# Kernel tuning notes

Hardware: AMD Instinct MI355X
Metric: run time of the kernel (lower is better)

Reference implementation:

```python
import jax, jax.numpy as jnp
import numpy as np

NUM_HEADS = 12

def setup_inputs() -> dict:
    key = jax.random.key(0)
    k1, k2 = jax.random.split(key)
    X = jax.random.normal(k1, (2, 2048, 768), dtype=jnp.float32)
    # torch nn.Linear(dim, 2*dim, bias=False) weight has shape [2*dim, dim]
    W_qkv = jax.random.normal(k2, (1536, 768), dtype=jnp.float32) * (768 ** -0.5)
    return {"X": X, "W_qkv": W_qkv}

def reference(X, W_qkv):
    B, N, C = X.shape
    H = NUM_HEADS
    hd = C // H
    scale = hd ** -0.5
    # qkv: [B, N, 2, H, hd]
    qkv = (X @ W_qkv.T).reshape(B, N, 2, H, hd)
    q = jnp.transpose(qkv[:, :, 0], (0, 2, 1, 3))  # [B, H, N, hd]
    k = jnp.transpose(qkv[:, :, 1], (0, 2, 1, 3))  # [B, H, N, hd]
    attn = jnp.einsum('bhnd,bhmd->bhnm', q, k) * scale  # [B, H, N, N]
    # dropout p=0 -> identity; double sum over heads and keys
    scores = attn.sum(axis=1).sum(axis=-1)  # [B, N]
    return scores
```

## Files before the change

### kernel.cpp

```cpp
#include <hip/hip_runtime.h>


#define DIM 768
#define BATCH 2
#define SEQ 2048


__global__ void colsum_part(const float* __restrict__ X, float* __restrict__ part) {
    int b  = blockIdx.x >> 6;
    int ch = blockIdx.x & 63;
    int i  = threadIdx.x;
    const float4* base = (const float4*)(X + ((size_t)b * SEQ + (size_t)ch * 32) * DIM) + i;
    float4 a = {0.f, 0.f, 0.f, 0.f};
    #pragma unroll 8
    for (int n = 0; n < 32; ++n) {
        float4 x = base[n * 192];
        a.x += x.x; a.y += x.y; a.z += x.z; a.w += x.w;
    }
    ((float4*)(part + (size_t)(b * 64 + ch) * DIM))[i] = a;
}

__global__ void v_kernel(const float* __restrict__ W, const float* __restrict__ part,
                         float* __restrict__ v) {
    __shared__ alignas(16) float xs[DIM];
    int bi = blockIdx.x;
    int b = bi >= 48;
    int tid = threadIdx.x;
    for (int d = tid; d < DIM; d += 256) {
        float s = 0.f;
        #pragma unroll 8
        for (int ch = 0; ch < 64; ++ch)
            s += part[(size_t)(b * 64 + ch) * DIM + d];
        xs[d] = s;
    }
    __syncthreads();
    int gw = bi * 4 + (tid >> 6);
    int lane = tid & 63;
    const float4* xs4 = (const float4*)xs;
    #pragma unroll
    for (int k = 0; k < 4; ++k) {
        int o = gw * 4 + k;
        int c = o - b * DIM;
        const float4* wr = (const float4*)(W + (size_t)(DIM + c) * DIM);
        float acc = 0.f;
        #pragma unroll
        for (int j = 0; j < 3; ++j) {
            float4 a = wr[lane + 64 * j];
            float4 s = xs4[lane + 64 * j];
            acc += a.x * s.x + a.y * s.y + a.z * s.z + a.w * s.w;
        }
        #pragma unroll
        for (int off = 32; off; off >>= 1)
            acc += __shfl_down(acc, off, 64);
        if (lane == 0) v[o] = acc;
    }
}

__global__ void t_part(const float* __restrict__ W, const float* __restrict__ v,
                       float* __restrict__ tp) {
    int bi = blockIdx.x;
    int b = bi / 24;
    int rem = bi % 24;
    int cs = rem / 3;
    int dch = rem % 3;
    int d = dch * 256 + threadIdx.x;
    const float* vb = v + b * DIM;
    float acc = 0.f;
    int c0 = cs * 96;
    #pragma unroll 8
    for (int c = c0; c < c0 + 96; ++c)
        acc += W[(size_t)c * DIM + d] * vb[c];
    tp[(size_t)(b * 8 + cs) * DIM + d] = acc;
}

__global__ void scores_k(const float* __restrict__ X, const float* __restrict__ tp,
                         float* __restrict__ out) {
    __shared__ alignas(16) float ft[DIM];
    int r0 = blockIdx.x * 4;
    int b = r0 >> 11;
    int tid = threadIdx.x;
    if (tid < 192) {
        const float4* base = (const float4*)(tp + (size_t)b * 8 * DIM) + tid;
        float4 s = {0.f, 0.f, 0.f, 0.f};
        #pragma unroll
        for (int cs = 0; cs < 8; ++cs) {
            float4 a = base[cs * 192];
            s.x += a.x; s.y += a.y; s.z += a.z; s.w += a.w;
        }
        ((float4*)ft)[tid] = s;
    }
    __syncthreads();
    int r = r0 + (tid >> 6);
    int lane = tid & 63;
    const float4* xr = (const float4*)(X + (size_t)r * DIM);
    const float4* t4 = (const float4*)ft;
    float acc = 0.f;
    #pragma unroll
    for (int j = 0; j < 3; ++j) {
        float4 a = xr[lane + 64 * j];
        float4 s = t4[lane + 64 * j];
        acc += a.x * s.x + a.y * s.y + a.z * s.z + a.w * s.w;
    }
    #pragma unroll
    for (int off = 32; off; off >>= 1)
        acc += __shfl_down(acc, off, 64);
    if (lane == 0) out[r] = acc * 0.125f;
}

extern "C" void kernel_launch(void* const* d_in, const int* in_sizes, int n_in,
                              void* d_out, int out_size, void* d_ws, size_t ws_size,
                              hipStream_t stream) {
    const float* X = (const float*)d_in[0];
    const float* W = (const float*)d_in[1];
    float* out = (float*)d_out;
    float* ws = (float*)d_ws;
    float* part = ws;
    float* v    = ws + 2 * 64 * DIM;
    float* tp   = v + 2 * DIM;

    colsum_part<<<128, 192, 0, stream>>>(X, part);
    v_kernel  <<<96, 256, 0, stream>>>(W, part, v);
    t_part    <<<48, 256, 0, stream>>>(W, v, tp);
    scores_k  <<<1024, 256, 0, stream>>>(X, tp, out);
}
```

Before: 86.44 us.

## Fuse four-stage scores pipeline into one cooperative kernel with grid syncs

Replaces the four separate kernel launches (column sum, v projection, t projection, per-row dot) with a single cooperative kernel of 512 blocks that separates the phases with grid.sync(). Work partitioning is also changed so more blocks take part in the column-sum and reduction stages. The aim is to remove launch gaps between the dependent small kernels and to spread the serial stages over more CUs. In exchange it pays for four grid-wide barriers, and it depends on all 512 blocks being co-resident.

```diff
diff --git a/kernel.cpp b/kernel.cpp
--- a/kernel.cpp
+++ b/kernel.cpp
@@ -1,110 +1,124 @@
 #include <hip/hip_runtime.h>
+#include <hip/hip_cooperative_groups.h>
+
+namespace cg = cooperative_groups;
 
 
 #define DIM 768
-#define BATCH 2
 #define SEQ 2048
+#define NBLK 512
 
 
-__global__ void colsum_part(const float* __restrict__ X, float* __restrict__ part) {
-    int b  = blockIdx.x >> 6;
-    int ch = blockIdx.x & 63;
-    int i  = threadIdx.x;
-    const float4* base = (const float4*)(X + ((size_t)b * SEQ + (size_t)ch * 32) * DIM) + i;
-    float4 a = {0.f, 0.f, 0.f, 0.f};
-    #pragma unroll 8
-    for (int n = 0; n < 32; ++n) {
-        float4 x = base[n * 192];
-        a.x += x.x; a.y += x.y; a.z += x.z; a.w += x.w;
+__global__ void __launch_bounds__(256, 2) fused_scores(
+    const float* __restrict__ X, const float* __restrict__ W,
+    float* __restrict__ out, float* __restrict__ ws)
+{
+    cg::grid_group grid = cg::this_grid();
+    __shared__ alignas(16) float sbuf[DIM];
+
+    float* part  = ws;
+    float* xsum  = ws + NBLK * DIM;
+    float* v     = xsum + 2 * DIM;
+    float* tpart = v + 2 * DIM;
+
+    const int bi   = blockIdx.x;
+    const int tid  = threadIdx.x;
+    const int lane = tid & 63;
+    const int wv   = tid >> 6;
+
+    if (tid < 192) {
+        const int b = bi >> 8;
+        const int chunk = bi & 255;
+        const float4* base = (const float4*)(X + ((size_t)b * SEQ + (size_t)chunk * 8) * DIM) + tid;
+        float4 a = {0.f, 0.f, 0.f, 0.f};
+        #pragma unroll
+        for (int n = 0; n < 8; ++n) {
+            float4 x = base[n * 192];
+            a.x += x.x; a.y += x.y; a.z += x.z; a.w += x.w;
+        }
+        ((float4*)(part + (size_t)bi * DIM))[tid] = a;
     }
-    ((float4*)(part + (size_t)(b * 64 + ch) * DIM))[i] = a;
-}
+    grid.sync();
 
-__global__ void v_kernel(const float* __restrict__ W, const float* __restrict__ part,
-                         float* __restrict__ v) {
-    __shared__ alignas(16) float xs[DIM];
-    int bi = blockIdx.x;
-    int b = bi >= 48;
-    int tid = threadIdx.x;
-    for (int d = tid; d < DIM; d += 256) {
-        float s = 0.f;
-        #pragma unroll 8
-        for (int ch = 0; ch < 64; ++ch)
-            s += part[(size_t)(b * 64 + ch) * DIM + d];
-        xs[d] = s;
+    if (bi < 384) {
+        int w = bi * 4 + wv;
+        int b = w / DIM;
+        int d = w - b * DIM;
+        const float* p = part + (size_t)(b * 256) * DIM + d;
+        float s = p[(size_t)lane * DIM] + p[(size_t)(lane + 64) * DIM]
+                + p[(size_t)(lane + 128) * DIM] + p[(size_t)(lane + 192) * DIM];
+        #pragma unroll
+        for (int off = 32; off; off >>= 1) s += __shfl_down(s, off, 64);
+        if (lane == 0) xsum[w] = s;
     }
-    __syncthreads();
-    int gw = bi * 4 + (tid >> 6);
-    int lane = tid & 63;
-    const float4* xs4 = (const float4*)xs;
-    #pragma unroll
-    for (int k = 0; k < 4; ++k) {
-        int o = gw * 4 + k;
-        int c = o - b * DIM;
+    grid.sync();
+
+    if (bi < 384) {
+        int w = bi * 4 + wv;
+        int b = w / DIM;
+        int c = w - b * DIM;
         const float4* wr = (const float4*)(W + (size_t)(DIM + c) * DIM);
+        const float4* xs = (const float4*)(xsum + b * DIM);
         float acc = 0.f;
         #pragma unroll
         for (int j = 0; j < 3; ++j) {
             float4 a = wr[lane + 64 * j];
-            float4 s = xs4[lane + 64 * j];
+            float4 s = xs[lane + 64 * j];
             acc += a.x * s.x + a.y * s.y + a.z * s.z + a.w * s.w;
         }
         #pragma unroll
-        for (int off = 32; off; off >>= 1)
-            acc += __shfl_down(acc, off, 64);
-        if (lane == 0) v[o] = acc;
+        for (int off = 32; off; off >>= 1) acc += __shfl_down(acc, off, 64);
+        if (lane == 0) v[w] = acc;
     }
-}
+    grid.sync();
 
-__global__ void t_part(const float* __restrict__ W, const float* __restrict__ v,
-                       float* __restrict__ tp) {
-    int bi = blockIdx.x;
-    int b = bi / 24;
-    int rem = bi % 24;
-    int cs = rem / 3;
-    int dch = rem % 3;
-    int d = dch * 256 + threadIdx.x;
-    const float* vb = v + b * DIM;
-    float acc = 0.f;
-    int c0 = cs * 96;
-    #pragma unroll 8
-    for (int c = c0; c < c0 + 96; ++c)
-        acc += W[(size_t)c * DIM + d] * vb[c];
-    tp[(size_t)(b * 8 + cs) * DIM + d] = acc;
-}
+    if (bi < 96) {
+        int cs  = bi / 6;
+        int r   = bi % 6;
+        int b   = r / 3;
+        int dch = r % 3;
+        int d   = dch * 256 + tid;
+        int c0  = cs * 48;
+        const float* vb = v + b * DIM;
+        float acc = 0.f;
+        #pragma unroll 8
+        for (int c = c0; c < c0 + 48; ++c)
+            acc += W[(size_t)c * DIM + d] * vb[c];
+        tpart[(size_t)(cs * 2 + b) * DIM + d] = acc;
+    }
+    grid.sync();
 
-__global__ void scores_k(const float* __restrict__ X, const float* __restrict__ tp,
-                         float* __restrict__ out) {
-    __shared__ alignas(16) float ft[DIM];
-    int r0 = blockIdx.x * 4;
-    int b = r0 >> 11;
-    int tid = threadIdx.x;
-    if (tid < 192) {
-        const float4* base = (const float4*)(tp + (size_t)b * 8 * DIM) + tid;
-        float4 s = {0.f, 0.f, 0.f, 0.f};
+    {
+        int b = bi >> 8;
+        if (tid < 192) {
+            const float4* tp4 = (const float4*)tpart;
+            float4 s = {0.f, 0.f, 0.f, 0.f};
+            #pragma unroll
+            for (int cs = 0; cs < 16; ++cs) {
+                float4 a = tp4[(cs * 2 + b) * 192 + tid];
+                s.x += a.x; s.y += a.y; s.z += a.z; s.w += a.w;
+            }
+            ((float4*)sbuf)[tid] = s;
+        }
+        __syncthreads();
+        const float4* t4 = (const float4*)sbuf;
+        int r0 = bi * 8 + wv * 2;
         #pragma unroll
-        for (int cs = 0; cs < 8; ++cs) {
-            float4 a = base[cs * 192];
-            s.x += a.x; s.y += a.y; s.z += a.z; s.w += a.w;
+        for (int rr = 0; rr < 2; ++rr) {
+            int rrow = r0 + rr;
+            const float4* xr = (const float4*)(X + (size_t)rrow * DIM);
+            float acc = 0.f;
+            #pragma unroll
+            for (int j = 0; j < 3; ++j) {
+                float4 a = xr[lane + 64 * j];
+                float4 s = t4[lane + 64 * j];
+                acc += a.x * s.x + a.y * s.y + a.z * s.z + a.w * s.w;
+            }
+            #pragma unroll
+            for (int off = 32; off; off >>= 1) acc += __shfl_down(acc, off, 64);
+            if (lane == 0) out[rrow] = acc * 0.125f;
         }
-        ((float4*)ft)[tid] = s;
     }
-    __syncthreads();
-    int r = r0 + (tid >> 6);
-    int lane = tid & 63;
-    const float4* xr = (const float4*)(X + (size_t)r * DIM);
-    const float4* t4 = (const float4*)ft;
-    float acc = 0.f;
-    #pragma unroll
-    for (int j = 0; j < 3; ++j) {
-        float4 a = xr[lane + 64 * j];
-        float4 s = t4[lane + 64 * j];
-        acc += a.x * s.x + a.y * s.y + a.z * s.z + a.w * s.w;
-    }
-    #pragma unroll
-    for (int off = 32; off; off >>= 1)
-        acc += __shfl_down(acc, off, 64);
-    if (lane == 0) out[r] = acc * 0.125f;
 }
 
 extern "C" void kernel_launch(void* const* d_in, const int* in_sizes, int n_in,
@@ -114,12 +128,8 @@
     const float* W = (const float*)d_in[1];
     float* out = (float*)d_out;
     float* ws = (float*)d_ws;
-    float* part = ws;
-    float* v    = ws + 2 * 64 * DIM;
-    float* tp   = v + 2 * DIM;
 
-    colsum_part<<<128, 192, 0, stream>>>(X, part);
-    v_kernel  <<<96, 256, 0, stream>>>(W, part, v);
-    t_part    <<<48, 256, 0, stream>>>(W, v, tp);
-    scores_k  <<<1024, 256, 0, stream>>>(X, tp, out);
+    void* args[] = { (void*)&X, (void*)&W, (void*)&out, (void*)&ws };
+    hipLaunchCooperativeKernel((const void*)fused_scores,
+                               dim3(NBLK), dim3(256), args, 0, stream);
 }
```

Measured after the change: 297.8 us. 3.45x slower.
